# Optimization experiments

Hardware: AMD Instinct MI355X
Metric: run time of the kernel (lower is better)

Reference implementation:

```python
import jax, jax.numpy as jnp
import numpy as np

N = 30000   # nodes
E = 120000  # edges
G = 512     # graphs in batch
F_IN = 1
H1 = 32
H2 = 64
NC = 10


def _lin_init(key, fan_in, fan_out):
    s = 1.0 / np.sqrt(fan_in)
    kw, kb = jax.random.split(key)
    w = jax.random.uniform(kw, (fan_in, fan_out), jnp.float32, minval=-s, maxval=s)
    b = jax.random.uniform(kb, (fan_out,), jnp.float32, minval=-s, maxval=s)
    return w, b


def setup_inputs() -> dict:
    key = jax.random.key(0)
    ks = jax.random.split(key, 16)
    inp = {}
    inp["x"] = jax.random.normal(ks[0], (N, F_IN), jnp.float32)
    inp["edge_attr"] = jax.random.uniform(ks[1], (E, 2), jnp.float32)
    inp["pos"] = jax.random.uniform(ks[2], (N, 2), jnp.float32) * 27.0
    inp["w1a"], inp["b1a"] = _lin_init(ks[3], 2, 25)
    inp["w1b"], inp["b1b"] = _lin_init(ks[4], 25, F_IN * H1)
    inp["root1"], inp["bias1"] = _lin_init(ks[5], F_IN, H1)
    inp["w2a"], inp["b2a"] = _lin_init(ks[6], 2, 25)
    inp["w2b"], inp["b2b"] = _lin_init(ks[7], 25, H1 * H2)
    inp["root2"], inp["bias2"] = _lin_init(ks[8], H1, H2)
    inp["fc1_w"], inp["fc1_b"] = _lin_init(ks[9], H2, 128)
    inp["fc2_w"], inp["fc2_b"] = _lin_init(ks[10], 128, NC)
    inp["edge_index"] = jax.random.randint(ks[11], (2, E), 0, N)
    inp["batch"] = jnp.sort(jax.random.randint(ks[12], (N,), 0, G))
    return inp


def _seg_mean(v, idx, n):
    s = jax.ops.segment_sum(v, idx, num_segments=n)
    c = jax.ops.segment_sum(jnp.ones((v.shape[0], 1), v.dtype), idx, num_segments=n)
    return s / jnp.maximum(c, 1.0)


def _nnconv(x, src, dst, ea, wa, ba, wb, bb, root, bias, n_seg, n_out):
    # per-edge weight matrix from edge MLP: [E, f_in, f_out]
    f_in, f_out = root.shape
    W = (jax.nn.relu(ea @ wa + ba) @ wb + bb).reshape(-1, f_in, f_out)
    msg = jnp.einsum('ei,eio->eo', x[src], W)          # gather + per-edge matmul
    aggr = _seg_mean(msg, dst, n_seg)[:n_out]          # mean scatter-reduce
    return aggr + x @ root + bias


def _forward(x, edge_attr, pos, w1a, b1a, w1b, b1b, root1, bias1,
             w2a, b2a, w2b, b2b, root2, bias2, fc1_w, fc1_b, fc2_w, fc2_b,
             edge_index, batch):
    row, col = edge_index[0], edge_index[1]
    h = jax.nn.elu(_nnconv(x, row, col, edge_attr, w1a, b1a, w1b, b1b,
                           root1, bias1, N, N))
    # graclus stand-in: fixed pairwise matching (consecutive cluster ids)
    n2 = N // 2
    cluster1 = jnp.arange(N) // 2
    x2 = jax.ops.segment_max(h, cluster1, num_segments=n2)     # max_pool x
    pos2 = _seg_mean(pos, cluster1, n2)                        # pool_pos (mean)
    batch2 = batch[0::2]                                       # pool_batch via perm
    row2 = cluster1[row]
    col2 = cluster1[col]
    mask = row2 != col2                                        # drop self loops
    col2m = jnp.where(mask, col2, n2)                          # route to dummy seg
    cart = (pos2[col2] - pos2[row2]) * mask[:, None]           # cartesian pseudo
    max_v = jnp.abs(cart).max()
    ea2 = cart / (2.0 * max_v) + 0.5
    h2 = jax.nn.elu(_nnconv(x2, row2, col2m, ea2, w2a, b2a, w2b, b2b,
                            root2, bias2, n2 + 1, n2))
    n3 = n2 // 2
    cluster2 = jnp.arange(n2) // 2
    x3 = jax.ops.segment_max(h2, cluster2, num_segments=n3)    # max_pool_x
    batch3 = batch2[0::2]
    g = _seg_mean(x3, batch3, G)                               # global_mean_pool
    g = jax.nn.elu(g @ fc1_w + fc1_b)                          # dropout off (eval)
    return jax.nn.log_softmax(g @ fc2_w + fc2_b, axis=1)


def reference(x, edge_attr, pos, w1a, b1a, w1b, b1b, root1, bias1,
              w2a, b2a, w2b, b2b, root2, bias2, fc1_w, fc1_b, fc2_w, fc2_b,
              edge_index, batch):
    return _forward(x, edge_attr, pos, w1a, b1a, w1b, b1b, root1, bias1,
                    w2a, b2a, w2b, b2b, root2, bias2, fc1_w, fc1_b,
                    fc2_w, fc2_b, edge_index, batch)
```

## Files before the change

### kernel.cpp

```cpp
#include <hip/hip_runtime.h>
#include <hip/hip_bf16.h>

#define N_NODES 30000
#define N_EDGES 120000
#define NGRAPH  512
#define N2      15000
#define N3      7500
#define NC      10

#define TSN   4
#define NTS   (N2 / TSN)
#define EC4   64
#define NB1   32
#define NBLK1 ((N_NODES + NB1 - 1) / NB1)
#define EC1   256
#define NDEGB ((N_EDGES + 255) / 256)

#define SC_C1 118
#define SC_CN 59
#define SC_C2 59
#define SC_CT (SC_C1 + SC_CN + SC_C2)

typedef __hip_bfloat16 bf16;

__device__ __forceinline__ float lo(const float* p, int i) { return p[i]; }
__device__ __forceinline__ float lo(const bf16* p, int i) { return __bfloat162float(p[i]); }
__device__ __forceinline__ void sto(float* p, int i, float v) { p[i] = v; }
__device__ __forceinline__ void sto(bf16* p, int i, float v) { p[i] = __float2bfloat16(v); }
__device__ __forceinline__ float elu(float x) { return x > 0.f ? x : expm1f(x); }
template <typename T> __host__ __device__ constexpr int want_flag() { return sizeof(T) == 4 ? 1 : 0; }

#define MV_OFF    0
#define GS_OFF    1
#define GC_OFF    32769
#define DEG1_OFF  33281
#define DEG2_OFF  63281
#define DEGN_OFF  78281
#define ZERO_FLOATS 93281
#define OFF1_OFF  93281
#define CUR1_OFF  123282
#define OFF2_OFF  153282
#define CUR2_OFF  168283
#define OFFN_OFF  183283
#define CURN_OFF  198284
#define BSUM_OFF  213284
#define ES1_OFF   213520
#define ESS_OFF   333520
#define DPOS_OFF  453520
#define X2_OFF    573520
#define P2_OFF    1053520
#define CT_OFF    1083520
#define MSG_OFF   1323520
#define FLAG_OFF  9003520

struct K1Smem {
  float srow[NB1][28];
  float axl[EC1], ayl[EC1], xsl[EC1];
  float w1a[50];
  float b1a[25];
  float b1b[32];
  float r1[32];
  float bs1[32];
  float hbuf[NB1][33];
  int offl[NB1 + 1];
};

struct K5Smem {
  float r2l[2048];
  float b2l[64];
  float hl[4][64];
};

__global__ __launch_bounds__(256) void kc_deg(
    const int* __restrict__ ei, const void* x, const void* ea, int* __restrict__ flag,
    int* __restrict__ deg1, int* __restrict__ deg2, int* __restrict__ degN) {
  if (blockIdx.x == NDEGB) {
    const bf16* xb = (const bf16*)x;
    const bf16* eb = (const bf16*)ea;
    int tid = threadIdx.x;
    float a = __bfloat162float(xb[tid]);
    float b = __bfloat162float(eb[tid]);
    int bad = (!(fabsf(a) < 1e3f)) || (!(fabsf(b) < 1e3f));
    unsigned long long m = __ballot(bad);
    __shared__ int anyb[4];
    int w = tid >> 6;
    if ((tid & 63) == 0) anyb[w] = (m != 0ULL) ? 1 : 0;
    __syncthreads();
    if (tid == 0) flag[0] = (anyb[0] | anyb[1] | anyb[2] | anyb[3]);
    return;
  }
  int e = blockIdx.x * 256 + threadIdx.x;
  if (e >= N_EDGES) return;
  int row = ei[e], col = ei[N_EDGES + e];
  atomicAdd(deg1 + col, 1);
  int r2 = row >> 1, c2 = col >> 1;
  if (r2 != c2) {
    atomicAdd(deg2 + c2, 1);
    atomicAdd(degN + r2, 1);
  }
}

__global__ __launch_bounds__(256) void ks_scanA(
    const int* __restrict__ deg1, const int* __restrict__ degN, const int* __restrict__ deg2,
    int* __restrict__ off1, int* __restrict__ offN, int* __restrict__ off2,
    int* __restrict__ bsum) {
  __shared__ int buf[256];
  int c = blockIdx.x, tid = threadIdx.x;
  const int* deg; int* off; int n, local;
  if (c < SC_C1)              { deg = deg1; off = off1; n = 30000; local = c; }
  else if (c < SC_C1 + SC_CN) { deg = degN; off = offN; n = 15000; local = c - SC_C1; }
  else                        { deg = deg2; off = off2; n = 15000; local = c - SC_C1 - SC_CN; }
  int i = local * 256 + tid;
  int v = (i < n) ? deg[i] : 0;
  buf[tid] = v;
  __syncthreads();
  for (int s = 1; s < 256; s <<= 1) {
    int t = (tid >= s) ? buf[tid - s] : 0;
    __syncthreads();
    buf[tid] += t;
    __syncthreads();
  }
  if (i <= n) off[i] = buf[tid] - v;
  if (tid == 255) bsum[c] = buf[255];
}

__global__ __launch_bounds__(256) void ks_scanB(int* __restrict__ bsum) {
  __shared__ int buf[256];
  int a = blockIdx.x, tid = threadIdx.x;
  int nc, cb;
  if (a == 0)      { nc = SC_C1; cb = 0; }
  else if (a == 1) { nc = SC_CN; cb = SC_C1; }
  else             { nc = SC_C2; cb = SC_C1 + SC_CN; }
  int v = (tid < nc) ? bsum[cb + tid] : 0;
  buf[tid] = v;
  __syncthreads();
  for (int s = 1; s < 256; s <<= 1) {
    int t = (tid >= s) ? buf[tid - s] : 0;
    __syncthreads();
    buf[tid] += t;
    __syncthreads();
  }
  if (tid < nc) bsum[cb + tid] = buf[tid] - v;
}

__global__ __launch_bounds__(256) void ks_scanC(
    int* __restrict__ off1, int* __restrict__ offN, int* __restrict__ off2,
    int* __restrict__ cur1, int* __restrict__ curN, int* __restrict__ cur2,
    const int* __restrict__ bsum) {
  int c = blockIdx.x, tid = threadIdx.x;
  int* off; int* cur; int n, local;
  if (c < SC_C1)              { off = off1; cur = cur1; n = 30000; local = c; }
  else if (c < SC_C1 + SC_CN) { off = offN; cur = curN; n = 15000; local = c - SC_C1; }
  else                        { off = off2; cur = cur2; n = 15000; local = c - SC_C1 - SC_CN; }
  int add = bsum[c];
  int i = local * 256 + tid;
  if (i <= n) off[i] += add;
  if (i < n) cur[i] = off[i];
}

__global__ __launch_bounds__(256) void kc_place(const int* __restrict__ ei,
                                                int* __restrict__ cur1, int* __restrict__ es1,
                                                int* __restrict__ cur2, int* __restrict__ dpos,
                                                int* __restrict__ curN, int* __restrict__ ess) {
  int e = blockIdx.x * 256 + threadIdx.x;
  if (e >= N_EDGES) return;
  int row = ei[e], col = ei[N_EDGES + e];
  int p = atomicAdd(cur1 + col, 1);
  es1[p] = e;
  int r2 = row >> 1, c2 = col >> 1;
  if (r2 != c2) {
    int q = atomicAdd(cur2 + c2, 1);
    dpos[e] = q;
    int u = atomicAdd(curN + r2, 1);
    ess[u] = e;
  }
}

template <typename T>
__device__ void k1_impl(K1Smem& S,
    const T* __restrict__ x, const T* __restrict__ ea, const T* __restrict__ pos,
    const int* __restrict__ ei,
    const T* __restrict__ w1a, const T* __restrict__ b1a,
    const T* __restrict__ w1b, const T* __restrict__ b1b,
    const T* __restrict__ root1, const T* __restrict__ bias1,
    const int* __restrict__ off1, const int* __restrict__ es1,
    float* __restrict__ x2, float* __restrict__ pos2) {
  int tid = threadIdx.x, t = blockIdx.x;
  int n0 = t * NB1;
  for (int j = tid; j < 50; j += 256) S.w1a[j] = lo(w1a, j);
  for (int j = tid; j < 25; j += 256) S.b1a[j] = lo(b1a, j);
  if (tid < 32) {
    S.b1b[tid] = lo(b1b, tid);
    S.r1[tid] = lo(root1, tid);
    S.bs1[tid] = lo(bias1, tid);
  }
  if (tid <= NB1) {
    int n = n0 + tid; if (n > N_NODES) n = N_NODES;
    S.offl[tid] = off1[n];
  }
  int half = tid >> 5, lk = tid & 31;
  float wreg[28];
#pragma unroll
  for (int k = 0; k < 25; ++k) wreg[k] = lo(w1b, k * 32 + lk);
  wreg[26] = 0.f; wreg[27] = 0.f;
  __syncthreads();
  wreg[25] = S.b1b[lk];
  float wa0 = 0.f, wa1 = 0.f, wb = 0.f;
  if (lk < 25) { wa0 = S.w1a[lk]; wa1 = S.w1a[25 + lk]; wb = S.b1a[lk]; }
  int jbeg = S.offl[0], jend = S.offl[NB1];
  int base = half * 4;
  float s0 = 0.f, s1 = 0.f, s2 = 0.f, s3 = 0.f;
  for (int jb = jbeg; jb < jend; jb += EC1) {
    int ecnt = jend - jb; if (ecnt > EC1) ecnt = EC1;
    __syncthreads();
    if (tid < ecnt) {
      int e = es1[jb + tid];
      S.axl[tid] = lo(ea, 2 * e);
      S.ayl[tid] = lo(ea, 2 * e + 1);
      S.xsl[tid] = lo(x, ei[e]);
    }
    __syncthreads();
    int je = jb + ecnt;
#define K1ACC(i, sacc) { \
    int lj = S.offl[base + i]; if (lj < jb) lj = jb; \
    int hj = S.offl[base + i + 1]; if (hj > je) hj = je; \
    for (int j = lj; j < hj; ++j) { \
      int sj = j - jb; \
      float tk = (lk < 25) ? fmaxf(S.axl[sj] * wa0 + S.ayl[sj] * wa1 + wb, 0.f) : 1.f; \
      sacc += S.xsl[sj] * tk; } }
    K1ACC(0, s0) K1ACC(1, s1) K1ACC(2, s2) K1ACC(3, s3)
#undef K1ACC
  }
  if (lk < 26) {
    S.srow[base][lk] = s0; S.srow[base + 1][lk] = s1;
    S.srow[base + 2][lk] = s2; S.srow[base + 3][lk] = s3;
  } else if (lk < 28) {
    S.srow[base][lk] = 0.f; S.srow[base + 1][lk] = 0.f;
    S.srow[base + 2][lk] = 0.f; S.srow[base + 3][lk] = 0.f;
  }
#pragma unroll
  for (int i = 0; i < 4; ++i) {
    int nl = base + i, n = n0 + nl;
    if (n < N_NODES) {
      const float4* sq = (const float4*)S.srow[nl];
      float a0 = 0.f, a1 = 0.f, a2 = 0.f, a3 = 0.f;
#pragma unroll
      for (int q = 0; q < 7; ++q) {
        float4 sv = sq[q];
        a0 += sv.x * wreg[4 * q];     a1 += sv.y * wreg[4 * q + 1];
        a2 += sv.z * wreg[4 * q + 2]; a3 += sv.w * wreg[4 * q + 3];
      }
      float c = (float)(S.offl[nl + 1] - S.offl[nl]);
      c = fmaxf(c, 1.f);
      S.hbuf[nl][lk] = elu(((a0 + a1) + (a2 + a3)) / c + lo(x, n) * S.r1[lk] + S.bs1[lk]);
    }
  }
  __syncthreads();
  for (int idx = tid; idx < (NB1 / 2) * 32; idx += 256) {
    int pl = idx >> 5, oo = idx & 31;
    int m = t * (NB1 / 2) + pl;
    if (m < N2)
      x2[m * 32 + oo] = fmaxf(S.hbuf[2 * pl][oo], S.hbuf[2 * pl + 1][oo]);
  }
  if (tid < NB1) {
    int pl = tid >> 1, c = tid & 1;
    int m = t * (NB1 / 2) + pl;
    if (m < N2)
      pos2[m * 2 + c] = 0.5f * (lo(pos, (2 * m) * 2 + c) + lo(pos, (2 * m + 1) * 2 + c));
  }
}

__global__ __launch_bounds__(256, 4) void k1_both(
    const int* __restrict__ flag,
    const void* x, const void* ea, const void* pos, const int* ei,
    const void* w1a, const void* b1a, const void* w1b, const void* b1b,
    const void* root1, const void* bias1,
    const int* off1, const int* es1, float* x2, float* pos2) {
  extern __shared__ char sm1[];
  K1Smem& S = *reinterpret_cast<K1Smem*>(sm1);
  if (flag[0] == 1)
    k1_impl<float>(S, (const float*)x, (const float*)ea, (const float*)pos, ei,
                   (const float*)w1a, (const float*)b1a, (const float*)w1b, (const float*)b1b,
                   (const float*)root1, (const float*)bias1, off1, es1, x2, pos2);
  else
    k1_impl<bf16>(S, (const bf16*)x, (const bf16*)ea, (const bf16*)pos, ei,
                  (const bf16*)w1a, (const bf16*)b1a, (const bf16*)w1b, (const bf16*)b1b,
                  (const bf16*)root1, (const bf16*)bias1, off1, es1, x2, pos2);
}

__global__ __launch_bounds__(256) void k3_cart(
    const int* __restrict__ ei, const float* __restrict__ pos2,
    float* __restrict__ cart, unsigned int* __restrict__ maxv) {
  int e = blockIdx.x * 256 + threadIdx.x;
  float m = 0.f;
  if (e < N_EDGES) {
    int r2 = ei[e] >> 1, c2 = ei[N_EDGES + e] >> 1;
    float cx = 0.f, cy = 0.f;
    if (r2 != c2) {
      cx = pos2[2 * c2] - pos2[2 * r2];
      cy = pos2[2 * c2 + 1] - pos2[2 * r2 + 1];
    }
    cart[2 * e] = cx;
    cart[2 * e + 1] = cy;
    m = fmaxf(fabsf(cx), fabsf(cy));
  }
#pragma unroll
  for (int s = 32; s > 0; s >>= 1)
    m = fmaxf(m, __shfl_xor(m, s, 64));
  __shared__ float wm[4];
  int lane = threadIdx.x & 63, wid = threadIdx.x >> 6;
  if (lane == 0) wm[wid] = m;
  __syncthreads();
  if (threadIdx.x == 0) {
    float mm = fmaxf(fmaxf(wm[0], wm[1]), fmaxf(wm[2], wm[3]));
    atomicMax(maxv, __float_as_uint(mm));
  }
}

template <typename T>
__global__ __launch_bounds__(256, 4) void k4_src(
    const int* __restrict__ flag,
    const int* __restrict__ ei, const float* __restrict__ cart, const float* __restrict__ maxv_f,
    const float* __restrict__ x2,
    const T* __restrict__ w2a, const T* __restrict__ b2a,
    const T* __restrict__ w2b, const T* __restrict__ b2b,
    const int* __restrict__ offN, const int* __restrict__ ess,
    const int* __restrict__ dpos,
    float* __restrict__ msg) {
  if (flag[0] != want_flag<T>()) return;
  __shared__ float Y[TSN][26][64];
  __shared__ __align__(16) float tl[EC4][32];
  __shared__ float xl[TSN][32];
  __shared__ float w2a_l[50];
  __shared__ float b2a_l[25];
  __shared__ float axl[EC4], ayl[EC4];
  __shared__ int dpl[EC4], nll[EC4];
  int tid = threadIdx.x, t = blockIdx.x;
  int n0 = t * TSN;
  if (tid < TSN * 32) xl[tid >> 5][tid & 31] = x2[n0 * 32 + tid];
  for (int j = tid; j < 50; j += 256) w2a_l[j] = lo(w2a, j);
  for (int j = tid; j < 25; j += 256) b2a_l[j] = lo(b2a, j);
  __syncthreads();
  int w = tid >> 6, o = tid & 63;
  {
    float acc[7][4];
#pragma unroll
    for (int s = 0; s < 7; ++s) {
      acc[s][0] = 0.f; acc[s][1] = 0.f; acc[s][2] = 0.f; acc[s][3] = 0.f;
    }
#pragma unroll 4
    for (int i = 0; i < 32; ++i) {
      float x0 = xl[0][i], x1 = xl[1][i], x2v = xl[2][i], x3 = xl[3][i];
#pragma unroll
      for (int s = 0; s < 7; ++s) {
        int kk = w + 4 * s;
        if (kk < 26) {
          const T* srcp = (kk < 25) ? (w2b + kk * 2048) : b2b;
          float q = lo(srcp, i * 64 + o);
          acc[s][0] += x0 * q; acc[s][1] += x1 * q;
          acc[s][2] += x2v * q; acc[s][3] += x3 * q;
        }
      }
    }
#pragma unroll
    for (int s = 0; s < 7; ++s) {
      int kk = w + 4 * s;
      if (kk < 26) {
        Y[0][kk][o] = acc[s][0]; Y[1][kk][o] = acc[s][1];
        Y[2][kk][o] = acc[s][2]; Y[3][kk][o] = acc[s][3];
      }
    }
  }
  float inv = 0.5f / maxv_f[0];
  int j0 = offN[n0], j1 = offN[n0 + TSN];
  float yreg[26];
  int cur_nl = -1;
  for (int jb = j0; jb < j1; jb += EC4) {
    int ecnt = j1 - jb; if (ecnt > EC4) ecnt = EC4;
    __syncthreads();
    if (tid < ecnt) {
      int e = ess[jb + tid];
      int r2 = ei[e] >> 1;
      nll[tid] = r2 & (TSN - 1);
      dpl[tid] = dpos[e];
      axl[tid] = cart[2 * e] * inv + 0.5f;
      ayl[tid] = cart[2 * e + 1] * inv + 0.5f;
    }
    __syncthreads();
    for (int idx = tid; idx < ecnt * 32; idx += 256) {
      int j = idx >> 5, k = idx & 31;
      if (k < 25)
        tl[j][k] = fmaxf(axl[j] * w2a_l[k] + ayl[j] * w2a_l[25 + k] + b2a_l[k], 0.f);
      else
        tl[j][k] = (k == 25) ? 1.f : 0.f;
    }
    __syncthreads();
    int slo = (ecnt * w) >> 2;
    int shi = (ecnt * (w + 1)) >> 2;
    for (int sj = slo; sj < shi; ++sj) {
      int nl = nll[sj];
      if (nl != cur_nl) {
        cur_nl = nl;
#pragma unroll
        for (int k = 0; k < 26; ++k) yreg[k] = Y[nl][k][o];
      }
      const float4* tq = (const float4*)tl[sj];
      float a0 = 0.f, a1 = 0.f, a2 = 0.f, a3 = 0.f;
      float4 tv;
      tv = tq[0]; a0 += tv.x * yreg[0];  a1 += tv.y * yreg[1];  a2 += tv.z * yreg[2];  a3 += tv.w * yreg[3];
      tv = tq[1]; a0 += tv.x * yreg[4];  a1 += tv.y * yreg[5];  a2 += tv.z * yreg[6];  a3 += tv.w * yreg[7];
      tv = tq[2]; a0 += tv.x * yreg[8];  a1 += tv.y * yreg[9];  a2 += tv.z * yreg[10]; a3 += tv.w * yreg[11];
      tv = tq[3]; a0 += tv.x * yreg[12]; a1 += tv.y * yreg[13]; a2 += tv.z * yreg[14]; a3 += tv.w * yreg[15];
      tv = tq[4]; a0 += tv.x * yreg[16]; a1 += tv.y * yreg[17]; a2 += tv.z * yreg[18]; a3 += tv.w * yreg[19];
      tv = tq[5]; a0 += tv.x * yreg[20]; a1 += tv.y * yreg[21]; a2 += tv.z * yreg[22]; a3 += tv.w * yreg[23];
      tv = tq[6]; a0 += tv.x * yreg[24]; a1 += tv.y * yreg[25];
      msg[(size_t)dpl[sj] * 64 + o] = (a0 + a1) + (a2 + a3);
    }
  }
}

template <typename T>
__device__ void k5_impl(K5Smem& S,
    const float* __restrict__ msg, const int* __restrict__ off2,
    const float* __restrict__ x2,
    const T* __restrict__ root2, const T* __restrict__ bias2,
    const int* __restrict__ batch,
    float* __restrict__ gsum, float* __restrict__ gcnt) {
  int tid = threadIdx.x;
  for (int j = tid; j < 2048; j += 256) S.r2l[j] = lo(root2, j);
  if (tid < 64) S.b2l[tid] = lo(bias2, tid);
  __syncthreads();
  int w = tid >> 6, o = tid & 63;
  int d = blockIdx.x * 4 + w;
  int j0 = off2[d], j1 = off2[d + 1];
  float s0 = 0.f, s1 = 0.f;
  int j = j0;
  for (; j + 1 < j1; j += 2) {
    s0 += msg[(size_t)j * 64 + o];
    s1 += msg[(size_t)(j + 1) * 64 + o];
  }
  if (j < j1) s0 += msg[(size_t)j * 64 + o];
  float c = fmaxf((float)(j1 - j0), 1.f);
  float r = S.b2l[o];
  const float* xr = x2 + d * 32;
#pragma unroll 8
  for (int i = 0; i < 32; ++i) r += xr[i] * S.r2l[i * 64 + o];
  S.hl[w][o] = elu((s0 + s1) / c + r);
  __syncthreads();
  if (tid < 128) {
    int p = tid >> 6, oo = tid & 63;
    float v = fmaxf(S.hl[2 * p][oo], S.hl[2 * p + 1][oo]);
    int m = blockIdx.x * 2 + p;
    int g = batch[4 * m];
    atomicAdd(gsum + g * 64 + oo, v);
    if (oo == 0) atomicAdd(gcnt + g, 1.f);
  }
}

__global__ __launch_bounds__(256) void k5_both(
    const int* __restrict__ flag,
    const float* msg, const int* off2, const float* x2,
    const void* root2, const void* bias2, const int* batch,
    float* gsum, float* gcnt) {
  extern __shared__ char sm5[];
  K5Smem& S = *reinterpret_cast<K5Smem*>(sm5);
  if (flag[0] == 1)
    k5_impl<float>(S, msg, off2, x2, (const float*)root2, (const float*)bias2, batch, gsum, gcnt);
  else
    k5_impl<bf16>(S, msg, off2, x2, (const bf16*)root2, (const bf16*)bias2, batch, gsum, gcnt);
}

template <typename T>
__device__ void k7_impl(const float* __restrict__ gsum, const float* __restrict__ gcnt,
                        const T* __restrict__ fc1_w, const T* __restrict__ fc1_b,
                        const T* __restrict__ fc2_w, const T* __restrict__ fc2_b,
                        T* __restrict__ out) {
  __shared__ float gv[64];
  __shared__ float h1s[128];
  __shared__ float zs[NC];
  __shared__ float lse;
  int g = blockIdx.x, tid = threadIdx.x;
  if (tid < 64) gv[tid] = gsum[g * 64 + tid] / fmaxf(gcnt[g], 1.f);
  __syncthreads();
  float a = lo(fc1_b, tid);
#pragma unroll 8
  for (int o = 0; o < 64; ++o) a += gv[o] * lo(fc1_w, o * 128 + tid);
  h1s[tid] = elu(a);
  __syncthreads();
  if (tid < NC) {
    float s = lo(fc2_b, tid);
    for (int j = 0; j < 128; ++j) s += h1s[j] * lo(fc2_w, j * NC + tid);
    zs[tid] = s;
  }
  __syncthreads();
  if (tid == 0) {
    float m = -1e30f;
    for (int c = 0; c < NC; ++c) m = fmaxf(m, zs[c]);
    float s = 0.f;
    for (int c = 0; c < NC; ++c) s += expf(zs[c] - m);
    lse = m + logf(s);
  }
  __syncthreads();
  if (tid < NC) sto(out, g * NC + tid, zs[tid] - lse);
}

__global__ __launch_bounds__(128) void k7_both(
    const int* __restrict__ flag,
    const float* gsum, const float* gcnt,
    const void* fc1_w, const void* fc1_b, const void* fc2_w, const void* fc2_b,
    void* out) {
  if (flag[0] == 1)
    k7_impl<float>(gsum, gcnt, (const float*)fc1_w, (const float*)fc1_b,
                   (const float*)fc2_w, (const float*)fc2_b, (float*)out);
  else
    k7_impl<bf16>(gsum, gcnt, (const bf16*)fc1_w, (const bf16*)fc1_b,
                  (const bf16*)fc2_w, (const bf16*)fc2_b, (bf16*)out);
}

extern "C" void kernel_launch(void* const* d_in, const int* in_sizes, int n_in,
                              void* d_out, int out_size, void* d_ws, size_t ws_size,
                              hipStream_t stream) {
  float* ws = (float*)d_ws;
  const int* flag = (const int*)(ws + FLAG_OFF);
  const int* ei = (const int*)d_in[19];
  const int* batch = (const int*)d_in[20];

  hipMemsetAsync(d_ws, 0, (size_t)ZERO_FLOATS * 4, stream);

  kc_deg<<<NDEGB + 1, 256, 0, stream>>>(
      ei, d_in[0], d_in[1], (int*)(ws + FLAG_OFF),
      (int*)(ws + DEG1_OFF), (int*)(ws + DEG2_OFF), (int*)(ws + DEGN_OFF));
  ks_scanA<<<SC_CT, 256, 0, stream>>>(
      (const int*)(ws + DEG1_OFF), (const int*)(ws + DEGN_OFF), (const int*)(ws + DEG2_OFF),
      (int*)(ws + OFF1_OFF), (int*)(ws + OFFN_OFF), (int*)(ws + OFF2_OFF),
      (int*)(ws + BSUM_OFF));
  ks_scanB<<<3, 256, 0, stream>>>((int*)(ws + BSUM_OFF));
  ks_scanC<<<SC_CT, 256, 0, stream>>>(
      (int*)(ws + OFF1_OFF), (int*)(ws + OFFN_OFF), (int*)(ws + OFF2_OFF),
      (int*)(ws + CUR1_OFF), (int*)(ws + CURN_OFF), (int*)(ws + CUR2_OFF),
      (const int*)(ws + BSUM_OFF));
  kc_place<<<NDEGB, 256, 0, stream>>>(
      ei, (int*)(ws + CUR1_OFF), (int*)(ws + ES1_OFF),
      (int*)(ws + CUR2_OFF), (int*)(ws + DPOS_OFF),
      (int*)(ws + CURN_OFF), (int*)(ws + ESS_OFF));

  k1_both<<<NBLK1, 256, sizeof(K1Smem), stream>>>(
      flag, d_in[0], d_in[1], d_in[2], ei,
      d_in[3], d_in[4], d_in[5], d_in[6], d_in[7], d_in[8],
      (const int*)(ws + OFF1_OFF), (const int*)(ws + ES1_OFF),
      ws + X2_OFF, ws + P2_OFF);

  k3_cart<<<NDEGB, 256, 0, stream>>>(
      ei, ws + P2_OFF, ws + CT_OFF, (unsigned int*)(ws + MV_OFF));

  k4_src<float><<<NTS, 256, 0, stream>>>(
      flag, ei, ws + CT_OFF, ws + MV_OFF, ws + X2_OFF,
      (const float*)d_in[9], (const float*)d_in[10], (const float*)d_in[11], (const float*)d_in[12],
      (const int*)(ws + OFFN_OFF), (const int*)(ws + ESS_OFF),
      (const int*)(ws + DPOS_OFF), ws + MSG_OFF);
  k4_src<bf16><<<NTS, 256, 0, stream>>>(
      flag, ei, ws + CT_OFF, ws + MV_OFF, ws + X2_OFF,
      (const bf16*)d_in[9], (const bf16*)d_in[10], (const bf16*)d_in[11], (const bf16*)d_in[12],
      (const int*)(ws + OFFN_OFF), (const int*)(ws + ESS_OFF),
      (const int*)(ws + DPOS_OFF), ws + MSG_OFF);

  k5_both<<<N2 / 4, 256, sizeof(K5Smem), stream>>>(
      flag, ws + MSG_OFF, (const int*)(ws + OFF2_OFF), ws + X2_OFF,
      d_in[13], d_in[14], batch, ws + GS_OFF, ws + GC_OFF);

  k7_both<<<NGRAPH, 128, 0, stream>>>(
      flag, ws + GS_OFF, ws + GC_OFF,
      d_in[15], d_in[16], d_in[17], d_in[18], d_out);
}
```

Before: 310.5 us.

## Merge k4 dtype launches and vectorize per-node weight contraction with shuffle reduction

Replaces the two templated k4_src launches, each of which exited early on the dtype flag, with one k4_both kernel that dispatches on the flag at runtime through dynamic shared memory. The per-node Y = x·W2b precompute now has each lane load four contiguous weights with one vector load and split the input-channel dimension across four lane groups, combining the partial sums with xor shuffles. This removes one kernel launch and cuts the number of global weight loads, at the cost of extra shuffle work and higher register pressure.

```diff
diff --git a/kernel.cpp b/kernel.cpp
--- a/kernel.cpp
+++ b/kernel.cpp
@@ -28,7 +28,15 @@
 __device__ __forceinline__ void sto(float* p, int i, float v) { p[i] = v; }
 __device__ __forceinline__ void sto(bf16* p, int i, float v) { p[i] = __float2bfloat16(v); }
 __device__ __forceinline__ float elu(float x) { return x > 0.f ? x : expm1f(x); }
-template <typename T> __host__ __device__ constexpr int want_flag() { return sizeof(T) == 4 ? 1 : 0; }
+
+__device__ __forceinline__ float b2f(unsigned short u) {
+  return __uint_as_float(((unsigned int)u) << 16);
+}
+__device__ __forceinline__ float4 lo4(const float* p) { return *(const float4*)p; }
+__device__ __forceinline__ float4 lo4(const bf16* p) {
+  ushort4 v = *(const ushort4*)p;
+  return make_float4(b2f(v.x), b2f(v.y), b2f(v.z), b2f(v.w));
+}
 
 #define MV_OFF    0
 #define GS_OFF    1
@@ -65,6 +73,16 @@
   int offl[NB1 + 1];
 };
 
+struct K4Smem {
+  float Y[TSN][26][64];
+  __align__(16) float tl[EC4][32];
+  float xl[TSN][32];
+  float w2a[50];
+  float b2a[25];
+  float axl[EC4], ayl[EC4];
+  int dpl[EC4], nll[EC4];
+};
+
 struct K5Smem {
   float r2l[2048];
   float b2l[64];
@@ -318,8 +336,7 @@
 }
 
 template <typename T>
-__global__ __launch_bounds__(256, 4) void k4_src(
-    const int* __restrict__ flag,
+__device__ void k4_impl(K4Smem& S,
     const int* __restrict__ ei, const float* __restrict__ cart, const float* __restrict__ maxv_f,
     const float* __restrict__ x2,
     const T* __restrict__ w2a, const T* __restrict__ b2a,
@@ -327,47 +344,46 @@
     const int* __restrict__ offN, const int* __restrict__ ess,
     const int* __restrict__ dpos,
     float* __restrict__ msg) {
-  if (flag[0] != want_flag<T>()) return;
-  __shared__ float Y[TSN][26][64];
-  __shared__ __align__(16) float tl[EC4][32];
-  __shared__ float xl[TSN][32];
-  __shared__ float w2a_l[50];
-  __shared__ float b2a_l[25];
-  __shared__ float axl[EC4], ayl[EC4];
-  __shared__ int dpl[EC4], nll[EC4];
   int tid = threadIdx.x, t = blockIdx.x;
   int n0 = t * TSN;
-  if (tid < TSN * 32) xl[tid >> 5][tid & 31] = x2[n0 * 32 + tid];
-  for (int j = tid; j < 50; j += 256) w2a_l[j] = lo(w2a, j);
-  for (int j = tid; j < 25; j += 256) b2a_l[j] = lo(b2a, j);
+  if (tid < TSN * 32) S.xl[tid >> 5][tid & 31] = x2[n0 * 32 + tid];
+  for (int j = tid; j < 50; j += 256) S.w2a[j] = lo(w2a, j);
+  for (int j = tid; j < 25; j += 256) S.b2a[j] = lo(b2a, j);
   __syncthreads();
   int w = tid >> 6, o = tid & 63;
   {
-    float acc[7][4];
-#pragma unroll
-    for (int s = 0; s < 7; ++s) {
-      acc[s][0] = 0.f; acc[s][1] = 0.f; acc[s][2] = 0.f; acc[s][3] = 0.f;
-    }
-#pragma unroll 4
-    for (int i = 0; i < 32; ++i) {
-      float x0 = xl[0][i], x1 = xl[1][i], x2v = xl[2][i], x3 = xl[3][i];
-#pragma unroll
-      for (int s = 0; s < 7; ++s) {
-        int kk = w + 4 * s;
-        if (kk < 26) {
-          const T* srcp = (kk < 25) ? (w2b + kk * 2048) : b2b;
-          float q = lo(srcp, i * 64 + o);
-          acc[s][0] += x0 * q; acc[s][1] += x1 * q;
-          acc[s][2] += x2v * q; acc[s][3] += x3 * q;
-        }
-      }
-    }
-#pragma unroll
+    int og = o & 15, ig = o >> 4;
     for (int s = 0; s < 7; ++s) {
       int kk = w + 4 * s;
-      if (kk < 26) {
-        Y[0][kk][o] = acc[s][0]; Y[1][kk][o] = acc[s][1];
-        Y[2][kk][o] = acc[s][2]; Y[3][kk][o] = acc[s][3];
+      if (kk >= 26) break;
+      const T* srcp = (kk < 25) ? (w2b + kk * 2048) : b2b;
+      float4 a0 = make_float4(0.f, 0.f, 0.f, 0.f), a1 = a0, a2 = a0, a3 = a0;
+#pragma unroll
+      for (int it = 0; it < 8; ++it) {
+        int i = it * 4 + ig;
+        float4 wv = lo4(srcp + i * 64 + og * 4);
+        float x0 = S.xl[0][i], x1 = S.xl[1][i], x2v = S.xl[2][i], x3 = S.xl[3][i];
+        a0.x += x0 * wv.x; a0.y += x0 * wv.y; a0.z += x0 * wv.z; a0.w += x0 * wv.w;
+        a1.x += x1 * wv.x; a1.y += x1 * wv.y; a1.z += x1 * wv.z; a1.w += x1 * wv.w;
+        a2.x += x2v * wv.x; a2.y += x2v * wv.y; a2.z += x2v * wv.z; a2.w += x2v * wv.w;
+        a3.x += x3 * wv.x; a3.y += x3 * wv.y; a3.z += x3 * wv.z; a3.w += x3 * wv.w;
+      }
+#pragma unroll
+      for (int mk = 16; mk <= 32; mk <<= 1) {
+        a0.x += __shfl_xor(a0.x, mk, 64); a0.y += __shfl_xor(a0.y, mk, 64);
+        a0.z += __shfl_xor(a0.z, mk, 64); a0.w += __shfl_xor(a0.w, mk, 64);
+        a1.x += __shfl_xor(a1.x, mk, 64); a1.y += __shfl_xor(a1.y, mk, 64);
+        a1.z += __shfl_xor(a1.z, mk, 64); a1.w += __shfl_xor(a1.w, mk, 64);
+        a2.x += __shfl_xor(a2.x, mk, 64); a2.y += __shfl_xor(a2.y, mk, 64);
+        a2.z += __shfl_xor(a2.z, mk, 64); a2.w += __shfl_xor(a2.w, mk, 64);
+        a3.x += __shfl_xor(a3.x, mk, 64); a3.y += __shfl_xor(a3.y, mk, 64);
+        a3.z += __shfl_xor(a3.z, mk, 64); a3.w += __shfl_xor(a3.w, mk, 64);
+      }
+      if (ig == 0) {
+        *(float4*)&S.Y[0][kk][og * 4] = a0;
+        *(float4*)&S.Y[1][kk][og * 4] = a1;
+        *(float4*)&S.Y[2][kk][og * 4] = a2;
+        *(float4*)&S.Y[3][kk][og * 4] = a3;
       }
     }
   }
@@ -381,30 +397,30 @@
     if (tid < ecnt) {
       int e = ess[jb + tid];
       int r2 = ei[e] >> 1;
-      nll[tid] = r2 & (TSN - 1);
-      dpl[tid] = dpos[e];
-      axl[tid] = cart[2 * e] * inv + 0.5f;
-      ayl[tid] = cart[2 * e + 1] * inv + 0.5f;
+      S.nll[tid] = r2 & (TSN - 1);
+      S.dpl[tid] = dpos[e];
+      S.axl[tid] = cart[2 * e] * inv + 0.5f;
+      S.ayl[tid] = cart[2 * e + 1] * inv + 0.5f;
     }
     __syncthreads();
     for (int idx = tid; idx < ecnt * 32; idx += 256) {
       int j = idx >> 5, k = idx & 31;
       if (k < 25)
-        tl[j][k] = fmaxf(axl[j] * w2a_l[k] + ayl[j] * w2a_l[25 + k] + b2a_l[k], 0.f);
+        S.tl[j][k] = fmaxf(S.axl[j] * S.w2a[k] + S.ayl[j] * S.w2a[25 + k] + S.b2a[k], 0.f);
       else
-        tl[j][k] = (k == 25) ? 1.f : 0.f;
+        S.tl[j][k] = (k == 25) ? 1.f : 0.f;
     }
     __syncthreads();
     int slo = (ecnt * w) >> 2;
     int shi = (ecnt * (w + 1)) >> 2;
     for (int sj = slo; sj < shi; ++sj) {
-      int nl = nll[sj];
+      int nl = S.nll[sj];
       if (nl != cur_nl) {
         cur_nl = nl;
 #pragma unroll
-        for (int k = 0; k < 26; ++k) yreg[k] = Y[nl][k][o];
+        for (int k = 0; k < 26; ++k) yreg[k] = S.Y[nl][k][o];
       }
-      const float4* tq = (const float4*)tl[sj];
+      const float4* tq = (const float4*)S.tl[sj];
       float a0 = 0.f, a1 = 0.f, a2 = 0.f, a3 = 0.f;
       float4 tv;
       tv = tq[0]; a0 += tv.x * yreg[0];  a1 += tv.y * yreg[1];  a2 += tv.z * yreg[2];  a3 += tv.w * yreg[3];
@@ -414,9 +430,24 @@
       tv = tq[4]; a0 += tv.x * yreg[16]; a1 += tv.y * yreg[17]; a2 += tv.z * yreg[18]; a3 += tv.w * yreg[19];
       tv = tq[5]; a0 += tv.x * yreg[20]; a1 += tv.y * yreg[21]; a2 += tv.z * yreg[22]; a3 += tv.w * yreg[23];
       tv = tq[6]; a0 += tv.x * yreg[24]; a1 += tv.y * yreg[25];
-      msg[(size_t)dpl[sj] * 64 + o] = (a0 + a1) + (a2 + a3);
+      msg[(size_t)S.dpl[sj] * 64 + o] = (a0 + a1) + (a2 + a3);
     }
   }
+}
+
+__global__ __launch_bounds__(256, 4) void k4_both(
+    const int* __restrict__ flag,
+    const int* ei, const float* cart, const float* maxv_f, const float* x2,
+    const void* w2a, const void* b2a, const void* w2b, const void* b2b,
+    const int* offN, const int* ess, const int* dpos, float* msg) {
+  extern __shared__ char sm4[];
+  K4Smem& S = *reinterpret_cast<K4Smem*>(sm4);
+  if (flag[0] == 1)
+    k4_impl<float>(S, ei, cart, maxv_f, x2, (const float*)w2a, (const float*)b2a,
+                   (const float*)w2b, (const float*)b2b, offN, ess, dpos, msg);
+  else
+    k4_impl<bf16>(S, ei, cart, maxv_f, x2, (const bf16*)w2a, (const bf16*)b2a,
+                  (const bf16*)w2b, (const bf16*)b2b, offN, ess, dpos, msg);
 }
 
 template <typename T>
@@ -553,14 +584,9 @@
   k3_cart<<<NDEGB, 256, 0, stream>>>(
       ei, ws + P2_OFF, ws + CT_OFF, (unsigned int*)(ws + MV_OFF));
 
-  k4_src<float><<<NTS, 256, 0, stream>>>(
+  k4_both<<<NTS, 256, sizeof(K4Smem), stream>>>(
       flag, ei, ws + CT_OFF, ws + MV_OFF, ws + X2_OFF,
-      (const float*)d_in[9], (const float*)d_in[10], (const float*)d_in[11], (const float*)d_in[12],
-      (const int*)(ws + OFFN_OFF), (const int*)(ws + ESS_OFF),
-      (const int*)(ws + DPOS_OFF), ws + MSG_OFF);
-  k4_src<bf16><<<NTS, 256, 0, stream>>>(
-      flag, ei, ws + CT_OFF, ws + MV_OFF, ws + X2_OFF,
-      (const bf16*)d_in[9], (const bf16*)d_in[10], (const bf16*)d_in[11], (const bf16*)d_in[12],
+      d_in[9], d_in[10], d_in[11], d_in[12],
       (const int*)(ws + OFFN_OFF), (const int*)(ws + ESS_OFF),
       (const int*)(ws + DPOS_OFF), ws + MSG_OFF);
 
```

After: 276.9 us. 10.8% less time.
